# Performance work log

Hardware: AMD Instinct MI355X
Metric: run time of the kernel (lower is better)

Reference implementation:

```python
import jax, jax.numpy as jnp
import numpy as np

B, CLN, QL, IH, IW = 64, 32, 32, 16, 16
CDF, SL = 256, 128
IDF = CLN * IH * IW  # 8192


def setup_inputs() -> dict:
    key = jax.random.key(0)
    k1, k2, k3 = jax.random.split(key, 3)
    inp = jax.random.normal(k1, (B, CLN, QL, IH, IW), dtype=jnp.float32)
    context = jax.random.normal(k2, (B, CDF, SL), dtype=jnp.float32)
    # Conv2d(cdf, idf, 1, bias=False) weight, squeezed to [idf, cdf]
    W = jax.random.normal(k3, (IDF, CDF), dtype=jnp.float32) * (1.0 / np.sqrt(CDF))
    return {"input": inp, "context": context, "W": W}


def reference(input, context, W):
    b, cln, queryL, ih, iw = input.shape
    idf = cln * ih * iw
    sourceL = context.shape[2]
    # target: b x queryL x (cln*ih*iw)
    targetT = jnp.transpose(input, (0, 2, 1, 3, 4)).reshape(b, queryL, idf)
    # 1x1 conv projection of context: b x idf x sourceL
    sourceT = jnp.einsum('oc,bcs->bos', W, context)
    # attention scores and softmax over sourceL (nn.Softmax on 2D -> dim=1)
    attn = jnp.einsum('bqd,bds->bqs', targetT, sourceT)  # b x queryL x sourceL
    attn = jax.nn.softmax(attn, axis=-1)
    attnT = jnp.transpose(attn, (0, 2, 1))  # b x sourceL x queryL
    # weighted context: b x idf x queryL
    wc = jnp.einsum('bds,bsq->bdq', sourceT, attnT)
    # faithful to torch .view: raw row-major reinterpretation of [b, idf, queryL]
    wc = wc.reshape(b, queryL, cln, ih, iw)
    wc = jnp.transpose(wc, (0, 2, 1, 3, 4))  # b x cln x queryL x ih x iw
    return (wc, attnT)
```

## Files before the change

kernel.cpp:

```cpp
#include <hip/hip_runtime.h>
#include <math.h>


#define ZK 16

typedef _Float16 f16x8 __attribute__((ext_vector_type(8)));
typedef __fp16 h16x2 __attribute__((ext_vector_type(2)));
typedef float f32x4 __attribute__((ext_vector_type(4)));

#define GLDS16(gp, lp)                                                          \
    __builtin_amdgcn_global_load_lds(                                           \
        (const __attribute__((address_space(1))) void*)(gp),                    \
        (__attribute__((address_space(3))) void*)(lp), 16, 0, 0)

__global__ __launch_bounds__(256) void k0a_prep(const float* __restrict__ Wm,
                                                _Float16* __restrict__ Wth,
                                                _Float16* __restrict__ Wtl) {
    const int kb = blockIdx.x;
    const int t = threadIdx.x;
    __shared__ float tile[32][260];
    {
        const int r = t >> 3;
        const int c0 = (t & 7) * 32;
        const float* src = Wm + (long)(kb * 32 + r) * 256 + c0;
#pragma unroll
        for (int i = 0; i < 8; ++i) {
            float4 v = *(const float4*)(src + i * 4);
            tile[r][c0 + i * 4 + 0] = v.x;
            tile[r][c0 + i * 4 + 1] = v.y;
            tile[r][c0 + i * 4 + 2] = v.z;
            tile[r][c0 + i * 4 + 3] = v.w;
        }
    }
    __syncthreads();
    const int lane = t & 63;
    const int quad = lane >> 4, l15 = lane & 15;
#pragma unroll
    for (int i = 0; i < 4; ++i) {
        int nsub = (t >> 6) * 4 + i;
        f16x8 oh, ol;
#pragma unroll
        for (int j = 0; j < 8; ++j) {
            float f = tile[quad * 8 + j][nsub * 16 + l15];
            _Float16 h = (_Float16)f;
            oh[j] = h;
            ol[j] = (_Float16)(f - (float)h);
        }
        long addr = ((long)(kb * 16 + nsub) * 64 + lane) * 8;
        *(f16x8*)(Wth + addr) = oh;
        *(f16x8*)(Wtl + addr) = ol;
    }
}

__global__ __launch_bounds__(256) void k0b_prep(const float* __restrict__ Wm,
                                                _Float16* __restrict__ Wbf) {
    const int t = threadIdx.x;
    const int fid = blockIdx.x * 4 + (t >> 6);
    const int mb = fid >> 3, kb4 = fid & 7;
    const int lane = t & 63;
    const int quad = lane >> 4, l15 = lane & 15;
    const float* src = Wm + (long)(mb * 16 + l15) * 256 + kb4 * 32 + quad * 8;
    float4 u0 = *(const float4*)(src);
    float4 u1 = *(const float4*)(src + 4);
    f16x8 o;
    o[0] = (_Float16)u0.x; o[1] = (_Float16)u0.y;
    o[2] = (_Float16)u0.z; o[3] = (_Float16)u0.w;
    o[4] = (_Float16)u1.x; o[5] = (_Float16)u1.y;
    o[6] = (_Float16)u1.z; o[7] = (_Float16)u1.w;
    *(f16x8*)(Wbf + ((long)fid * 64 + lane) * 8) = o;
}

__global__ __launch_bounds__(256, 2) void k1_mfma(const float* __restrict__ inp,
                                                  const _Float16* __restrict__ Wth,
                                                  const _Float16* __restrict__ Wtl,
                                                  float* __restrict__ tWpart) {
    const int kz = blockIdx.x;
    const int m0 = blockIdx.y * 64;
    const int t = threadIdx.x;
    const int lane = t & 63, wv = t >> 6;
    const int quad = lane >> 4, l15 = lane & 15;

    __shared__ _Float16 Fh[2][4][64][8];
    __shared__ _Float16 Fl[2][4][64][8];

    const float* arow;
    {
        const int mA = m0 + (t >> 2);
        arow = inp + (long)(mA >> 5) * 262144 + (long)(mA & 31) * 256 + (t & 3) * 8;
    }
    _Float16* wh = &Fh[0][t >> 6][((t & 3) << 4) | ((t >> 2) & 15)][0];
    _Float16* wl = &Fl[0][t >> 6][((t & 3) << 4) | ((t >> 2) & 15)][0];

    f32x4 acc[4][4];
#pragma unroll
    for (int i = 0; i < 4; ++i)
#pragma unroll
        for (int j = 0; j < 4; ++j) acc[i][j] = (f32x4){0.f, 0.f, 0.f, 0.f};

    float4 Ar[2][2];
    f16x8 Bh[2][4], Bl[2][4];

    {
        const int kg = kz * 512;
        const long off = (long)(kg >> 8) * 8192 + (kg & 255);
        Ar[0][0] = *(const float4*)(arow + off);
        Ar[0][1] = *(const float4*)(arow + off + 4);
        const long bb = ((long)((kz * 16) * 16 + wv * 4) * 64 + lane) * 8;
#pragma unroll
        for (int j = 0; j < 4; ++j) {
            Bh[0][j] = *(const f16x8*)(Wth + bb + (long)j * 512);
            Bl[0][j] = *(const f16x8*)(Wtl + bb + (long)j * 512);
        }
    }

#pragma unroll
    for (int it = 0; it < 16; ++it) {
        const int cur = it & 1, nxt = cur ^ 1;
        if (it < 15) {
            const int kg = kz * 512 + (it + 1) * 32;
            const long off = (long)(kg >> 8) * 8192 + (kg & 255);
            Ar[nxt][0] = *(const float4*)(arow + off);
            Ar[nxt][1] = *(const float4*)(arow + off + 4);
            const long bb = ((long)((kz * 16 + it + 1) * 16 + wv * 4) * 64 + lane) * 8;
#pragma unroll
            for (int j = 0; j < 4; ++j) {
                Bh[nxt][j] = *(const f16x8*)(Wth + bb + (long)j * 512);
                Bl[nxt][j] = *(const f16x8*)(Wtl + bb + (long)j * 512);
            }
        }
        __builtin_amdgcn_sched_barrier(0);

        {
            const float4 a0 = Ar[cur][0], a1 = Ar[cur][1];
            h16x2 h01 = __builtin_amdgcn_cvt_pkrtz(a0.x, a0.y);
            h16x2 h23 = __builtin_amdgcn_cvt_pkrtz(a0.z, a0.w);
            h16x2 h45 = __builtin_amdgcn_cvt_pkrtz(a1.x, a1.y);
            h16x2 h67 = __builtin_amdgcn_cvt_pkrtz(a1.z, a1.w);
            h16x2 l01 = __builtin_amdgcn_cvt_pkrtz(a0.x - (float)h01[0], a0.y - (float)h01[1]);
            h16x2 l23 = __builtin_amdgcn_cvt_pkrtz(a0.z - (float)h23[0], a0.w - (float)h23[1]);
            h16x2 l45 = __builtin_amdgcn_cvt_pkrtz(a1.x - (float)h45[0], a1.y - (float)h45[1]);
            h16x2 l67 = __builtin_amdgcn_cvt_pkrtz(a1.z - (float)h67[0], a1.w - (float)h67[1]);
            union { f16x8 v; h16x2 p[4]; } H, L;
            H.p[0] = h01; H.p[1] = h23; H.p[2] = h45; H.p[3] = h67;
            L.p[0] = l01; L.p[1] = l23; L.p[2] = l45; L.p[3] = l67;
            *(f16x8*)(wh + cur * 2048) = H.v;
            *(f16x8*)(wl + cur * 2048) = L.v;
        }
        asm volatile("s_waitcnt lgkmcnt(0)" ::: "memory");
        __builtin_amdgcn_sched_barrier(0);
        __builtin_amdgcn_s_barrier();
        __builtin_amdgcn_sched_barrier(0);

        f16x8 ah[4], al[4];
#pragma unroll
        for (int i = 0; i < 4; ++i) {
            ah[i] = *(const f16x8*)&Fh[cur][i][lane][0];
            al[i] = *(const f16x8*)&Fl[cur][i][lane][0];
        }
#pragma unroll
        for (int i = 0; i < 4; ++i)
#pragma unroll
            for (int j = 0; j < 4; ++j)
                acc[i][j] = __builtin_amdgcn_mfma_f32_16x16x32_f16(ah[i], Bh[cur][j], acc[i][j], 0, 0, 0);
#pragma unroll
        for (int i = 0; i < 4; ++i)
#pragma unroll
            for (int j = 0; j < 4; ++j)
                acc[i][j] = __builtin_amdgcn_mfma_f32_16x16x32_f16(al[i], Bh[cur][j], acc[i][j], 0, 0, 0);
#pragma unroll
        for (int i = 0; i < 4; ++i)
#pragma unroll
            for (int j = 0; j < 4; ++j)
                acc[i][j] = __builtin_amdgcn_mfma_f32_16x16x32_f16(ah[i], Bl[cur][j], acc[i][j], 0, 0, 0);
    }

    float* outp = tWpart + (long)kz * 524288;
#pragma unroll
    for (int i = 0; i < 4; ++i) {
        const int mbase = m0 + i * 16 + quad * 4;
#pragma unroll
        for (int j = 0; j < 4; ++j) {
            const int c = (wv * 4 + j) * 16 + l15;
#pragma unroll
            for (int rg = 0; rg < 4; ++rg)
                outp[(long)(mbase + rg) * 256 + c] = acc[i][j][rg];
        }
    }
}

__global__ __launch_bounds__(256) void k2_logits_softmax(const float* __restrict__ tWpart,
                                                         const float* __restrict__ ctx,
                                                         float* __restrict__ attnT) {
    const int qg = blockIdx.x;
    const int b  = blockIdx.y;
    const int t  = threadIdx.x;
    __shared__ float tw4[4][256];
#pragma unroll
    for (int qq = 0; qq < 4; ++qq) {
        const float* p = tWpart + (long)(b * 32 + qg * 4 + qq) * 256 + t;
        float s = 0.f;
#pragma unroll
        for (int z = 0; z < ZK; ++z) s += p[(long)z * 524288];
        tw4[qq][t] = s;
    }
    __syncthreads();
    const int q = t >> 6, lane = t & 63;
    const float* ctxb = ctx + (long)b * 32768 + lane * 2;
    float ax = 0.f, ay = 0.f;
#pragma unroll 4
    for (int c = 0; c < 256; ++c) {
        float tw = tw4[q][c];
        float2 cv = *(const float2*)(ctxb + c * 128);
        ax = fmaf(tw, cv.x, ax);
        ay = fmaf(tw, cv.y, ay);
    }
    float mx = fmaxf(ax, ay);
#pragma unroll
    for (int m = 1; m <= 32; m <<= 1) mx = fmaxf(mx, __shfl_xor(mx, m));
    float ex = expf(ax - mx);
    float ey = expf(ay - mx);
    float sm = ex + ey;
#pragma unroll
    for (int m = 1; m <= 32; m <<= 1) sm += __shfl_xor(sm, m);
    float inv = 1.f / sm;
    ex *= inv; ey *= inv;
    float* o = attnT + (long)b * 4096 + (qg * 4 + q);
    o[(lane * 2 + 0) * 32] = ex;
    o[(lane * 2 + 1) * 32] = ey;
}

__global__ __launch_bounds__(256) void k3_ctxA(const float* __restrict__ ctx,
                                               const float* __restrict__ attnT,
                                               _Float16* __restrict__ ctxAqf) {
    const int cg = blockIdx.x;
    const int b  = blockIdx.y;
    const int t  = threadIdx.x;
    __shared__ float at[128][32];
    __shared__ float cs[32][132];
#pragma unroll
    for (int i = 0; i < 4; ++i)
        *(float4*)((float*)at + i * 1024 + t * 4) =
            *(const float4*)(attnT + (long)b * 4096 + i * 1024 + t * 4);
#pragma unroll
    for (int i = 0; i < 4; ++i) {
        int idx = i * 256 + t;
        int c = idx >> 5, sseg = (idx & 31) * 4;
        *(float4*)&cs[c][sseg] = *(const float4*)(ctx + (long)b * 32768 + (long)(cg * 32 + c) * 128 + sseg);
    }
    __syncthreads();
    const int c = t >> 3;
    const int qs = (t & 7) * 4;
    float4 acc = make_float4(0.f, 0.f, 0.f, 0.f);
#pragma unroll 4
    for (int s = 0; s < 128; ++s) {
        float cv = cs[c][s];
        float4 av = *(const float4*)&at[s][qs];
        acc.x = fmaf(cv, av.x, acc.x);
        acc.y = fmaf(cv, av.y, acc.y);
        acc.z = fmaf(cv, av.z, acc.z);
        acc.w = fmaf(cv, av.w, acc.w);
    }
    const int cglob = cg * 32 + c;
    const long cpart = (long)(cglob >> 5) * 64 + 16 * ((cglob >> 3) & 3);
    float vals[4] = {acc.x, acc.y, acc.z, acc.w};
#pragma unroll
    for (int u = 0; u < 4; ++u) {
        int n = b * 32 + qs + u;
        long addr = ((long)(n >> 4) * 8 * 64 + cpart + (n & 15)) * 8 + (cglob & 7);
        ctxAqf[addr] = (_Float16)vals[u];
    }
}

__global__ __launch_bounds__(256) void k4_mfma(const _Float16* __restrict__ Wbf,
                                               const _Float16* __restrict__ ctxAqf,
                                               float* __restrict__ out0) {
    const int t = threadIdx.x;
    const int lane = t & 63, wv = t >> 6;
    const int mb = blockIdx.x * 4 + wv;
    const int nb0 = blockIdx.y * 8;

    __shared__ _Float16 Bs[32768];

    {
        const _Float16* gsrc = ctxAqf + (long)nb0 * 4096;
#pragma unroll
        for (int i = 0; i < 16; ++i) {
            const int chunk = i * 256 + wv * 64;
            GLDS16(gsrc + (long)chunk * 8 + lane * 8, Bs + chunk * 8);
        }
    }
    __syncthreads();

    const _Float16* abase = Wbf + ((long)mb * 8 * 64 + lane) * 8;

    f32x4 acc[8];
#pragma unroll
    for (int j = 0; j < 8; ++j) acc[j] = (f32x4){0.f, 0.f, 0.f, 0.f};

#pragma unroll
    for (int kb = 0; kb < 8; ++kb) {
        f16x8 af = *(const f16x8*)(abase + (long)kb * 512);
#pragma unroll
        for (int j = 0; j < 8; ++j) {
            f16x8 bf = *(const f16x8*)(Bs + (j * 8 + kb) * 512 + lane * 8);
            acc[j] = __builtin_amdgcn_mfma_f32_16x16x32_f16(af, bf, acc[j], 0, 0, 0);
        }
    }
    const int quad = lane >> 4, col = lane & 15;
#pragma unroll
    for (int j = 0; j < 8; ++j) {
        const int n = (nb0 + j) * 16 + col;
        float* ob = out0 + (long)(n >> 5) * 262144 + (n & 31);
#pragma unroll
        for (int rg = 0; rg < 4; ++rg) {
            const int d = mb * 16 + quad * 4 + rg;
            ob[(long)((d >> 3) & 31) * 8192 + (long)(d >> 8) * 256 + (long)(d & 7) * 32] = acc[j][rg];
        }
    }
}

extern "C" void kernel_launch(void* const* d_in, const int* in_sizes, int n_in,
                              void* d_out, int out_size, void* d_ws, size_t ws_size,
                              hipStream_t stream) {
    const float* inp = (const float*)d_in[0];
    const float* ctx = (const float*)d_in[1];
    const float* Wm  = (const float*)d_in[2];
    float* out0 = (float*)d_out;
    float* out1 = out0 + 16777216;

    float* wsf = (float*)d_ws;
    float* tWpart = wsf;
    _Float16* Wbf    = (_Float16*)wsf;
    _Float16* ctxAqf = (_Float16*)(wsf + 1048576);
    _Float16* Wth = (_Float16*)(wsf + 8388608);
    _Float16* Wtl = Wth + 2097152;

    hipLaunchKernelGGL(k0a_prep, dim3(256), dim3(256), 0, stream, Wm, Wth, Wtl);
    hipLaunchKernelGGL(k1_mfma, dim3(16, 32), dim3(256), 0, stream, inp, Wth, Wtl, tWpart);
    hipLaunchKernelGGL(k2_logits_softmax, dim3(8, 64), dim3(256), 0, stream, tWpart, ctx, out1);
    hipLaunchKernelGGL(k0b_prep, dim3(1024), dim3(256), 0, stream, Wm, Wbf);
    hipLaunchKernelGGL(k3_ctxA, dim3(8, 64), dim3(256), 0, stream, ctx, out1, ctxAqf);
    hipLaunchKernelGGL(k4_mfma, dim3(128, 16), dim3(256), 0, stream, Wbf, ctxAqf, out0);
}
```

Measured before the change: 207.3 us.

## Merge weight prep kernels, pad split-K stride, restructure logits softmax

Fuses the two weight conversion kernels into one launch when the workspace is large enough, giving each buffer its own region so the Wbf prep no longer has to wait for k2 to finish with the aliased tWpart. Pads the split-K partial stride to avoid cache/channel aliasing across z slices. Rewrites the logits/softmax kernel to use one block per (batch, query) with 128 threads, vectorised float2 partial reduction, and four accumulators, at the cost of more blocks and extra shared-memory reductions. A fallback path keeps the old layout when the workspace is small.

```diff
diff --git a/kernel.cpp b/kernel.cpp
--- a/kernel.cpp
+++ b/kernel.cpp
@@ -13,12 +13,10 @@
         (const __attribute__((address_space(1))) void*)(gp),                    \
         (__attribute__((address_space(3))) void*)(lp), 16, 0, 0)
 
-__global__ __launch_bounds__(256) void k0a_prep(const float* __restrict__ Wm,
-                                                _Float16* __restrict__ Wth,
-                                                _Float16* __restrict__ Wtl) {
-    const int kb = blockIdx.x;
-    const int t = threadIdx.x;
-    __shared__ float tile[32][260];
+__device__ __forceinline__ void k0a_body(const float* __restrict__ Wm,
+                                         _Float16* __restrict__ Wth,
+                                         _Float16* __restrict__ Wtl,
+                                         int kb, int t, float (*tile)[260]) {
     {
         const int r = t >> 3;
         const int c0 = (t & 7) * 32;
@@ -52,10 +50,10 @@
     }
 }
 
-__global__ __launch_bounds__(256) void k0b_prep(const float* __restrict__ Wm,
-                                                _Float16* __restrict__ Wbf) {
-    const int t = threadIdx.x;
-    const int fid = blockIdx.x * 4 + (t >> 6);
+__device__ __forceinline__ void k0b_body(const float* __restrict__ Wm,
+                                         _Float16* __restrict__ Wbf,
+                                         int bx, int t) {
+    const int fid = bx * 4 + (t >> 6);
     const int mb = fid >> 3, kb4 = fid & 7;
     const int lane = t & 63;
     const int quad = lane >> 4, l15 = lane & 15;
@@ -70,10 +68,30 @@
     *(f16x8*)(Wbf + ((long)fid * 64 + lane) * 8) = o;
 }
 
+__global__ __launch_bounds__(256) void k0a_prep(const float* __restrict__ Wm,
+                                                _Float16* __restrict__ Wth,
+                                                _Float16* __restrict__ Wtl) {
+    __shared__ float tile[32][260];
+    k0a_body(Wm, Wth, Wtl, blockIdx.x, threadIdx.x, tile);
+}
+__global__ __launch_bounds__(256) void k0b_prep(const float* __restrict__ Wm,
+                                                _Float16* __restrict__ Wbf) {
+    k0b_body(Wm, Wbf, blockIdx.x, threadIdx.x);
+}
+__global__ __launch_bounds__(256) void k0_all(const float* __restrict__ Wm,
+                                              _Float16* __restrict__ Wth,
+                                              _Float16* __restrict__ Wtl,
+                                              _Float16* __restrict__ Wbf) {
+    __shared__ float tile[32][260];
+    if (blockIdx.x < 256) k0a_body(Wm, Wth, Wtl, blockIdx.x, threadIdx.x, tile);
+    else                  k0b_body(Wm, Wbf, blockIdx.x - 256, threadIdx.x);
+}
+
 __global__ __launch_bounds__(256, 2) void k1_mfma(const float* __restrict__ inp,
                                                   const _Float16* __restrict__ Wth,
                                                   const _Float16* __restrict__ Wtl,
-                                                  float* __restrict__ tWpart) {
+                                                  float* __restrict__ tWpart,
+                                                  const long zstride) {
     const int kz = blockIdx.x;
     const int m0 = blockIdx.y * 64;
     const int t = threadIdx.x;
@@ -174,7 +192,7 @@
                 acc[i][j] = __builtin_amdgcn_mfma_f32_16x16x32_f16(ah[i], Bl[cur][j], acc[i][j], 0, 0, 0);
     }
 
-    float* outp = tWpart + (long)kz * 524288;
+    float* outp = tWpart + (long)kz * zstride;
 #pragma unroll
     for (int i = 0; i < 4; ++i) {
         const int mbase = m0 + i * 16 + quad * 4;
@@ -188,45 +206,53 @@
     }
 }
 
-__global__ __launch_bounds__(256) void k2_logits_softmax(const float* __restrict__ tWpart,
+__global__ __launch_bounds__(128) void k2_logits_softmax(const float* __restrict__ tWpart,
                                                          const float* __restrict__ ctx,
-                                                         float* __restrict__ attnT) {
-    const int qg = blockIdx.x;
-    const int b  = blockIdx.y;
-    const int t  = threadIdx.x;
-    __shared__ float tw4[4][256];
-#pragma unroll
-    for (int qq = 0; qq < 4; ++qq) {
-        const float* p = tWpart + (long)(b * 32 + qg * 4 + qq) * 256 + t;
-        float s = 0.f;
-#pragma unroll
-        for (int z = 0; z < ZK; ++z) s += p[(long)z * 524288];
-        tw4[qq][t] = s;
-    }
-    __syncthreads();
-    const int q = t >> 6, lane = t & 63;
-    const float* ctxb = ctx + (long)b * 32768 + lane * 2;
-    float ax = 0.f, ay = 0.f;
-#pragma unroll 4
-    for (int c = 0; c < 256; ++c) {
-        float tw = tw4[q][c];
-        float2 cv = *(const float2*)(ctxb + c * 128);
-        ax = fmaf(tw, cv.x, ax);
-        ay = fmaf(tw, cv.y, ay);
-    }
-    float mx = fmaxf(ax, ay);
+                                                         float* __restrict__ attnT,
+                                                         const long zstride) {
+    const int b = blockIdx.x;
+    const int q = blockIdx.y;
+    const int t = threadIdx.x;
+    __shared__ float tw[256];
+    __shared__ float red[4];
+    {
+        const float* p = tWpart + (long)(b * 32 + q) * 256 + t * 2;
+        float sx = 0.f, sy = 0.f;
+#pragma unroll
+        for (int z = 0; z < ZK; ++z) {
+            float2 v = *(const float2*)(p + (long)z * zstride);
+            sx += v.x; sy += v.y;
+        }
+        tw[t * 2] = sx;
+        tw[t * 2 + 1] = sy;
+    }
+    __syncthreads();
+    const float* ctxb = ctx + (long)b * 32768 + t;
+    float a0 = 0.f, a1 = 0.f, a2 = 0.f, a3 = 0.f;
+#pragma unroll 2
+    for (int c = 0; c < 256; c += 4) {
+        a0 = fmaf(tw[c + 0], ctxb[(c + 0) * 128], a0);
+        a1 = fmaf(tw[c + 1], ctxb[(c + 1) * 128], a1);
+        a2 = fmaf(tw[c + 2], ctxb[(c + 2) * 128], a2);
+        a3 = fmaf(tw[c + 3], ctxb[(c + 3) * 128], a3);
+    }
+    float ax = (a0 + a1) + (a2 + a3);
+    const int wv = t >> 6;
+    float mx = ax;
 #pragma unroll
     for (int m = 1; m <= 32; m <<= 1) mx = fmaxf(mx, __shfl_xor(mx, m));
+    if ((t & 63) == 0) red[wv] = mx;
+    __syncthreads();
+    mx = fmaxf(red[0], red[1]);
     float ex = expf(ax - mx);
-    float ey = expf(ay - mx);
-    float sm = ex + ey;
+    float sm = ex;
 #pragma unroll
     for (int m = 1; m <= 32; m <<= 1) sm += __shfl_xor(sm, m);
-    float inv = 1.f / sm;
-    ex *= inv; ey *= inv;
-    float* o = attnT + (long)b * 4096 + (qg * 4 + q);
-    o[(lane * 2 + 0) * 32] = ex;
-    o[(lane * 2 + 1) * 32] = ey;
+    if ((t & 63) == 0) red[2 + wv] = sm;
+    __syncthreads();
+    sm = red[2] + red[3];
+    ex *= (1.f / sm);
+    attnT[(long)b * 4096 + t * 32 + q] = ex;
 }
 
 __global__ __launch_bounds__(256) void k3_ctxA(const float* __restrict__ ctx,
@@ -328,17 +354,36 @@
     float* out0 = (float*)d_out;
     float* out1 = out0 + 16777216;
 
-    float* wsf = (float*)d_ws;
-    float* tWpart = wsf;
-    _Float16* Wbf    = (_Float16*)wsf;
-    _Float16* ctxAqf = (_Float16*)(wsf + 1048576);
-    _Float16* Wth = (_Float16*)(wsf + 8388608);
-    _Float16* Wtl = Wth + 2097152;
-
-    hipLaunchKernelGGL(k0a_prep, dim3(256), dim3(256), 0, stream, Wm, Wth, Wtl);
-    hipLaunchKernelGGL(k1_mfma, dim3(16, 32), dim3(256), 0, stream, inp, Wth, Wtl, tWpart);
-    hipLaunchKernelGGL(k2_logits_softmax, dim3(8, 64), dim3(256), 0, stream, tWpart, ctx, out1);
-    hipLaunchKernelGGL(k0b_prep, dim3(1024), dim3(256), 0, stream, Wm, Wbf);
-    hipLaunchKernelGGL(k3_ctxA, dim3(8, 64), dim3(256), 0, stream, ctx, out1, ctxAqf);
-    hipLaunchKernelGGL(k4_mfma, dim3(128, 16), dim3(256), 0, stream, Wbf, ctxAqf, out0);
-}
+    char* wsb = (char*)d_ws;
+    const size_t BIG_NEED = 47255552ull;
+
+    if (ws_size >= BIG_NEED) {
+        const long zs = 524288 + 1088;
+        float*    tWpart = (float*)wsb;
+        _Float16* Wth    = (_Float16*)(wsb + 33624064);
+        _Float16* Wtl    = (_Float16*)(wsb + 37818368);
+        _Float16* Wbf    = (_Float16*)(wsb + 42012672);
+        _Float16* ctxAqf = (_Float16*)(wsb + 46206976);
+
+        hipLaunchKernelGGL(k0_all, dim3(1280), dim3(256), 0, stream, Wm, Wth, Wtl, Wbf);
+        hipLaunchKernelGGL(k1_mfma, dim3(16, 32), dim3(256), 0, stream, inp, Wth, Wtl, tWpart, zs);
+        hipLaunchKernelGGL(k2_logits_softmax, dim3(64, 32), dim3(128), 0, stream, tWpart, ctx, out1, zs);
+        hipLaunchKernelGGL(k3_ctxA, dim3(8, 64), dim3(256), 0, stream, ctx, out1, ctxAqf);
+        hipLaunchKernelGGL(k4_mfma, dim3(128, 16), dim3(256), 0, stream, Wbf, ctxAqf, out0);
+    } else {
+        const long zs = 524288;
+        float* wsf = (float*)d_ws;
+        float*    tWpart = wsf;
+        _Float16* Wbf    = (_Float16*)wsf;
+        _Float16* ctxAqf = (_Float16*)(wsf + 1048576);
+        _Float16* Wth    = (_Float16*)(wsf + 8388608);
+        _Float16* Wtl    = Wth + 2097152;
+
+        hipLaunchKernelGGL(k0a_prep, dim3(256), dim3(256), 0, stream, Wm, Wth, Wtl);
+        hipLaunchKernelGGL(k1_mfma, dim3(16, 32), dim3(256), 0, stream, inp, Wth, Wtl, tWpart, zs);
+        hipLaunchKernelGGL(k2_logits_softmax, dim3(64, 32), dim3(128), 0, stream, tWpart, ctx, out1, zs);
+        hipLaunchKernelGGL(k0b_prep, dim3(1024), dim3(256), 0, stream, Wm, Wbf);
+        hipLaunchKernelGGL(k3_ctxA, dim3(8, 64), dim3(256), 0, stream, ctx, out1, ctxAqf);
+        hipLaunchKernelGGL(k4_mfma, dim3(128, 16), dim3(256), 0, stream, Wbf, ctxAqf, out0);
+    }
+}
```

Measured after the change: 190.4 us. -8.1%, faster.
